# Optimization experiments

Measured on AMD Instinct MI355X. Metric: run time of the kernel, lower is better.

The kernel has to match this reference:

```python
import jax, jax.numpy as jnp
import numpy as np

# NF4 codebook (bitsandbytes nf4 data type, 16 levels)
NF4_TABLE = np.array([
    -1.0, -0.6961928009986877, -0.5250730514526367, -0.39491748809814453,
    -0.28444138169288635, -0.18477343022823334, -0.09105003625154495, 0.0,
    0.07958029955625534, 0.16093020141124725, 0.24611230194568634,
    0.33791524171829224, 0.44070982933044434, 0.5626170039176941,
    0.7229568362236023, 1.0], dtype=np.float32)

BLOCKSIZE = 64
SCALING = 32.0 / 16.0  # lora_alpha / r


def setup_inputs() -> dict:
    key = jax.random.key(0)
    k1, k2, k3, k4, k5 = jax.random.split(key, 5)
    tokens, in_f, out_f, r = 256, 4096, 11008, 16
    x = jax.random.normal(k1, (tokens, in_f), dtype=jnp.float32)
    q_codes = jax.random.randint(k2, (out_f, in_f), 0, 16, dtype=jnp.int32)
    absmax = jax.random.uniform(k3, (out_f, in_f // BLOCKSIZE), dtype=jnp.float32)
    lora_A = jax.random.normal(k4, (r, in_f), dtype=jnp.float32) * (1.0 / np.sqrt(in_f))
    lora_B = jax.random.normal(k5, (out_f, r), dtype=jnp.float32) * 0.02
    return {"x": x, "q_codes": q_codes, "absmax": absmax,
            "lora_A": lora_A, "lora_B": lora_B}


def reference(x, q_codes, absmax, lora_A, lora_B):
    out_f, in_f = q_codes.shape
    nf4 = jnp.asarray(NF4_TABLE, dtype=x.dtype)
    # Dequantize: codebook lookup, then per-block absmax scale.
    W = nf4[q_codes].reshape(out_f, in_f // BLOCKSIZE, BLOCKSIZE)
    W = (W * absmax[:, :, None]).reshape(out_f, in_f)  # [out_f, in_f]
    # Base 4-bit linear (no bias in bnb Linear4bit default here).
    base = x @ W.T  # [tokens, out_f]
    # LoRA path: dropout p=0 is identity in eval; scaling = alpha/r.
    lora = (x @ lora_A.T) @ lora_B.T  # [tokens, r] -> [tokens, out_f]
    return base + lora * jnp.asarray(SCALING, dtype=x.dtype)
```

## Files before the change

kernel.cpp:

```cpp
#include <hip/hip_runtime.h>
#include <hip/hip_fp16.h>

typedef unsigned int uint;
typedef unsigned short ushort;

typedef __attribute__((ext_vector_type(8))) _Float16 f16x8;
typedef __attribute__((ext_vector_type(4))) float f32x4;

#define TOK 256
#define OUTF 11008
#define INF 4096
#define BM 256
#define BN 64
#define NT2 172

__device__ __constant__ float NF4_TBL[16] = {
    -1.0f, -0.6961928009986877f, -0.5250730514526367f, -0.39491748809814453f,
    -0.28444138169288635f, -0.18477343022823334f, -0.09105003625154495f, 0.0f,
    0.07958029955625534f, 0.16093020141124725f, 0.24611230194568634f,
    0.33791524171829224f, 0.44070982933044434f, 0.5626170039176941f,
    0.7229568362236023f, 1.0f};

__device__ __forceinline__ ushort f2h(float f) {
  return __half_as_ushort(__float2half(f));
}

__device__ __forceinline__ void async_cp16(const void* g, void* l) {
  __builtin_amdgcn_global_load_lds(
      (const __attribute__((address_space(1))) uint*)g,
      (__attribute__((address_space(3))) uint*)l, 16, 0, 0);
}

__device__ __forceinline__ float nf4v(int c, int tbits) {
  return __int_as_float(__builtin_amdgcn_ds_bpermute(c << 2, tbits));
}

__global__ void prep_kernel(const float4* __restrict__ x4, ushort4* __restrict__ xh4,
                            const float4* __restrict__ lB4, ushort4* __restrict__ lBh4,
                            const int4* __restrict__ qc4, uint* __restrict__ q4) {
  const int stride = gridDim.x * blockDim.x;
  const int t0 = blockIdx.x * blockDim.x + threadIdx.x;
  for (int i = t0; i < OUTF * (INF / 8); i += stride) {
    int4 a = qc4[(size_t)i * 2];
    int4 b = qc4[(size_t)i * 2 + 1];
    uint p = (uint)(a.x & 15) | ((uint)(a.y & 15) << 4) | ((uint)(a.z & 15) << 8) |
             ((uint)(a.w & 15) << 12) | ((uint)(b.x & 15) << 16) |
             ((uint)(b.y & 15) << 20) | ((uint)(b.z & 15) << 24) |
             ((uint)(b.w & 15) << 28);
    q4[i] = p;
  }
  for (int i = t0; i < TOK * INF / 4; i += stride) {
    float4 v = x4[i];
    ushort4 o;
    o.x = f2h(v.x); o.y = f2h(v.y); o.z = f2h(v.z); o.w = f2h(v.w);
    xh4[i] = o;
  }
  for (int i = t0; i < OUTF * 16; i += stride) {
    int n = i >> 4, jq = i & 15;
    ushort4 o = {0, 0, 0, 0};
    if (jq < 4) {
      float4 v = lB4[n * 4 + jq];
      o.x = f2h(v.x); o.y = f2h(v.y); o.z = f2h(v.z); o.w = f2h(v.w);
    }
    lBh4[i] = o;
  }
}

__global__ __launch_bounds__(1024)
void xa_kernel(const float* __restrict__ x, const float* __restrict__ lA,
               ushort* __restrict__ xa2) {
  const int m = blockIdx.x;
  const int t = threadIdx.x;
  const float4* x4 = (const float4*)(x + (size_t)m * INF);
  const float4* lA4 = (const float4*)lA;
  float4 xv = x4[t];
  float acc[16];
#pragma unroll
  for (int j = 0; j < 16; ++j) {
    float4 a = lA4[j * (INF / 4) + t];
    acc[j] = xv.x * a.x + xv.y * a.y + xv.z * a.z + xv.w * a.w;
  }
#pragma unroll
  for (int j = 0; j < 16; ++j)
#pragma unroll
    for (int s = 32; s > 0; s >>= 1) acc[j] += __shfl_xor(acc[j], s, 64);
  __shared__ float red[16][16];
  const int w = t >> 6, l = t & 63;
  if (l == 0) {
#pragma unroll
    for (int j = 0; j < 16; ++j) red[w][j] = acc[j];
  }
  __syncthreads();
  if (t < 64) {
    ushort v = 0;
    if (t < 16) {
      float s = 0.f;
#pragma unroll
      for (int w2 = 0; w2 < 16; ++w2) s += red[w2][t];
      v = f2h(2.0f * s);
    }
    xa2[m * 64 + t] = v;
  }
}

__global__ __launch_bounds__(256, 3)
void gemm_kernel(const uint* __restrict__ q4, const float* __restrict__ am,
                 const ushort* __restrict__ xh, const ushort* __restrict__ lBh,
                 const ushort* __restrict__ xa2, float* __restrict__ dest, int nst) {
  __shared__ ushort Abuf[BM * 64];
  __shared__ ushort Bbuf[64 * 64];
  __shared__ float Qax[1024];

  const int tid = threadIdx.x;
  const int w = tid >> 6;
  const int l = tid & 63;
  const int chunk = l >> 4;
  const int rlo = l & 15;
  const int split = blockIdx.x / NT2;
  const int ntile = blockIdx.x - split * NT2;
  const int n0 = ntile * BN;
  const int kb0 = split * nst;

  const int tbits = __float_as_int(NF4_TBL[l & 15]);

  const int arow = w * 8 + (l >> 3);
  const int acol = ((l & 7) ^ (l >> 3)) << 3;
  int aoff[2][4];
#pragma unroll
  for (int ks2 = 0; ks2 < 2; ++ks2) {
    const int cc = ks2 * 4 + chunk;
#pragma unroll
    for (int mt = 0; mt < 4; ++mt)
      aoff[ks2][mt] = (w * 64 + mt * 16 + rlo) * 64 + ((cc ^ (l & 7)) << 3);
  }

  const int qr = tid >> 2;
  const int oc2 = (tid & 3) << 1;
  const uint* qb = q4 + (size_t)(n0 + qr) * (INF / 8) + (size_t)kb0 * 8 + oc2;
  const int bd0 = qr * 64 + ((oc2 ^ (qr & 7)) << 3);
  const int bd1 = qr * 64 + (((oc2 + 1) ^ (qr & 7)) << 3);

  int boff[2][4];
#pragma unroll
  for (int ks2 = 0; ks2 < 2; ++ks2)
#pragma unroll
    for (int nt = 0; nt < 4; ++nt)
      boff[ks2][nt] = (nt * 16 + rlo) * 64 + (((ks2 * 4 + chunk) ^ (rlo & 7)) << 3);

  f32x4 acc[4][4];
#pragma unroll
  for (int mt = 0; mt < 4; ++mt)
#pragma unroll
    for (int nt = 0; nt < 4; ++nt) acc[mt][nt] = (f32x4){0.f, 0.f, 0.f, 0.f};

  if (w == 0) {
#pragma unroll
    for (int j = 0; j < 4; ++j)
      async_cp16(am + (size_t)(n0 + l) * 64 + kb0 + j * 4, (char*)Qax + j * 1024);
  }
#pragma unroll
  for (int i = 0; i < 8; ++i) {
    const ushort* g = xh + (size_t)(i * 32 + arow) * INF + kb0 * 64 + acol;
    async_cp16(g, &Abuf[(i * 256 + w * 64) * 8]);
  }
  uint2 qreg = *(const uint2*)qb;

  for (int s = 0; s < nst; ++s) {
    __syncthreads();

    const int sl = s & 15;
    const __half2 ax2 = __float2half2_rn(Qax[(sl >> 2) * 256 + qr * 4 + (sl & 3)]);
    {
      const uint q0 = qreg.x, q1 = qreg.y;
      union { __half2 h[4]; uint4 u; } r0, r1;
      r0.h[0] = __hmul2(__floats2half2_rn(nf4v(q0 & 15, tbits), nf4v((q0 >> 4) & 15, tbits)), ax2);
      r0.h[1] = __hmul2(__floats2half2_rn(nf4v((q0 >> 8) & 15, tbits), nf4v((q0 >> 12) & 15, tbits)), ax2);
      r0.h[2] = __hmul2(__floats2half2_rn(nf4v((q0 >> 16) & 15, tbits), nf4v((q0 >> 20) & 15, tbits)), ax2);
      r0.h[3] = __hmul2(__floats2half2_rn(nf4v((q0 >> 24) & 15, tbits), nf4v(q0 >> 28, tbits)), ax2);
      r1.h[0] = __hmul2(__floats2half2_rn(nf4v(q1 & 15, tbits), nf4v((q1 >> 4) & 15, tbits)), ax2);
      r1.h[1] = __hmul2(__floats2half2_rn(nf4v((q1 >> 8) & 15, tbits), nf4v((q1 >> 12) & 15, tbits)), ax2);
      r1.h[2] = __hmul2(__floats2half2_rn(nf4v((q1 >> 16) & 15, tbits), nf4v((q1 >> 20) & 15, tbits)), ax2);
      r1.h[3] = __hmul2(__floats2half2_rn(nf4v((q1 >> 24) & 15, tbits), nf4v(q1 >> 28, tbits)), ax2);
      *(uint4*)&Bbuf[bd0] = r0.u;
      *(uint4*)&Bbuf[bd1] = r1.u;
    }
    f16x8 areg[2][4];
#pragma unroll
    for (int ks2 = 0; ks2 < 2; ++ks2)
#pragma unroll
      for (int mt = 0; mt < 4; ++mt) areg[ks2][mt] = *(const f16x8*)&Abuf[aoff[ks2][mt]];

    __syncthreads();

    if (s + 1 < nst) {
      const int kb = kb0 + s + 1;
#pragma unroll
      for (int i = 0; i < 8; ++i) {
        const ushort* g = xh + (size_t)(i * 32 + arow) * INF + kb * 64 + acol;
        async_cp16(g, &Abuf[(i * 256 + w * 64) * 8]);
      }
      qreg = *(const uint2*)(qb + (s + 1) * 8);
      if (((s + 1) & 15) == 0 && w == 0) {
#pragma unroll
        for (int j = 0; j < 4; ++j)
          async_cp16(am + (size_t)(n0 + l) * 64 + kb0 + s + 1 + j * 4, (char*)Qax + j * 1024);
      }
    }

#pragma unroll
    for (int ks2 = 0; ks2 < 2; ++ks2) {
      f16x8 b[4];
#pragma unroll
      for (int nt = 0; nt < 4; ++nt) b[nt] = *(const f16x8*)&Bbuf[boff[ks2][nt]];
#pragma unroll
      for (int mt = 0; mt < 4; ++mt)
#pragma unroll
        for (int nt = 0; nt < 4; ++nt)
          acc[mt][nt] = __builtin_amdgcn_mfma_f32_16x16x32_f16(areg[ks2][mt], b[nt], acc[mt][nt], 0, 0, 0);
    }
  }

  if (split == 0) {
    f16x8 a_l[4], b_l[4];
#pragma unroll
    for (int mt = 0; mt < 4; ++mt)
      a_l[mt] = *(const f16x8*)(xa2 + (size_t)(w * 64 + mt * 16 + rlo) * 64 + chunk * 8);
#pragma unroll
    for (int nt = 0; nt < 4; ++nt)
      b_l[nt] = *(const f16x8*)(lBh + (size_t)(n0 + nt * 16 + rlo) * 64 + chunk * 8);
#pragma unroll
    for (int mt = 0; mt < 4; ++mt)
#pragma unroll
      for (int nt = 0; nt < 4; ++nt)
        acc[mt][nt] = __builtin_amdgcn_mfma_f32_16x16x32_f16(a_l[mt], b_l[nt], acc[mt][nt], 0, 0, 0);
  }

  float* dst = dest + (size_t)split * TOK * OUTF;
#pragma unroll
  for (int mt = 0; mt < 4; ++mt) {
#pragma unroll
    for (int nt = 0; nt < 4; ++nt) {
      int c = n0 + nt * 16 + rlo;
#pragma unroll
      for (int r = 0; r < 4; ++r) {
        int row = w * 64 + mt * 16 + chunk * 4 + r;
        dst[(size_t)row * OUTF + c] = acc[mt][nt][r];
      }
    }
  }
}

__global__ void reduce_kernel(const float4* __restrict__ part, float4* __restrict__ out,
                              int ks) {
  const int QN = TOK * OUTF / 4;
  int i = blockIdx.x * blockDim.x + threadIdx.x;
  if (i < QN) {
    float4 s = part[i];
    for (int s2 = 1; s2 < ks; ++s2) {
      float4 p = part[(size_t)s2 * QN + i];
      s.x += p.x; s.y += p.y; s.z += p.z; s.w += p.w;
    }
    out[i] = s;
  }
}

extern "C" void kernel_launch(void* const* d_in, const int* in_sizes, int n_in,
                              void* d_out, int out_size, void* d_ws, size_t ws_size,
                              hipStream_t stream) {
  const float* x = (const float*)d_in[0];
  const int* qc = (const int*)d_in[1];
  const float* am = (const float*)d_in[2];
  const float* lA = (const float*)d_in[3];
  const float* lB = (const float*)d_in[4];
  float* out = (float*)d_out;

  const size_t off_lB = (size_t)TOK * INF * 2;
  const size_t off_xa2 = off_lB + (size_t)OUTF * 64 * 2;
  const size_t off_q4 = off_xa2 + (size_t)TOK * 64 * 2;
  const size_t off_part = off_q4 + (size_t)OUTF * (INF / 8) * 4;
  const size_t part_bytes = (size_t)TOK * OUTF * 4;

  ushort* xh = (ushort*)d_ws;
  ushort* lBh = (ushort*)((char*)d_ws + off_lB);
  ushort* xa2 = (ushort*)((char*)d_ws + off_xa2);
  uint* q4 = (uint*)((char*)d_ws + off_q4);
  float* part = (float*)((char*)d_ws + off_part);

  int ks = 1;
  if (ws_size >= off_part + 4 * part_bytes) ks = 4;
  else if (ws_size >= off_part + 2 * part_bytes) ks = 2;
  float* dest = (ks == 1) ? out : part;

  prep_kernel<<<2048, 256, 0, stream>>>((const float4*)x, (ushort4*)xh,
                                        (const float4*)lB, (ushort4*)lBh,
                                        (const int4*)qc, q4);
  xa_kernel<<<TOK, 1024, 0, stream>>>(x, lA, xa2);
  gemm_kernel<<<NT2 * ks, 256, 0, stream>>>(q4, am, xh, lBh, xa2, dest, 64 / ks);
  if (ks > 1)
    reduce_kernel<<<(TOK * OUTF / 4 + 255) / 256, 256, 0, stream>>>((const float4*)part,
                                                                    (float4*)out, ks);
}
```

Before: 323.8 us.

## Pre-swizzle x into MFMA fragment order and double-buffer dequantized B tiles

The prep kernel now writes fp16 x in the exact per-lane MFMA fragment layout, so the GEMM loads A operands straight from global memory into registers. This removes the LDS A buffer and its async copies. The main loop is software-pipelined with two register sets for A and two LDS B buffers, so dequantizing the next tile overlaps with MFMA on the current one, and each step needs one lightweight barrier instead of two. All absmax values for the tile are loaded up front, and MFMA sections get raised priority. In exchange, register pressure rises (launch bounds drop to 2 waves), every A load goes to global memory or cache, and the absmax load ignores the kb0 offset when split > 0, which may be a correctness bug.

Measured after the change: 327.4 us. No clear change (+1.1%).

```diff
diff --git a/kernel.cpp b/kernel.cpp
--- a/kernel.cpp
+++ b/kernel.cpp
@@ -35,7 +35,12 @@
   return __int_as_float(__builtin_amdgcn_ds_bpermute(c << 2, tbits));
 }
 
-__global__ void prep_kernel(const float4* __restrict__ x4, ushort4* __restrict__ xh4,
+__device__ __forceinline__ void step_barrier() {
+  asm volatile("s_waitcnt lgkmcnt(0)" ::: "memory");
+  __builtin_amdgcn_s_barrier();
+}
+
+__global__ void prep_kernel(const float* __restrict__ x, uint4* __restrict__ xf4,
                             const float4* __restrict__ lB4, ushort4* __restrict__ lBh4,
                             const int4* __restrict__ qc4, uint* __restrict__ q4) {
   const int stride = gridDim.x * blockDim.x;
@@ -49,11 +54,21 @@
              ((uint)(b.w & 15) << 28);
     q4[i] = p;
   }
-  for (int i = t0; i < TOK * INF / 4; i += stride) {
-    float4 v = x4[i];
-    ushort4 o;
-    o.x = f2h(v.x); o.y = f2h(v.y); o.z = f2h(v.z); o.w = f2h(v.w);
-    xh4[i] = o;
+  for (int f = t0; f < TOK * INF / 8; f += stride) {
+    int l = f & 63;
+    int rlo = l & 15, chunk = l >> 4;
+    int ms = (f >> 6) & 7;
+    int mt = ms >> 1, ks2 = ms & 1;
+    int w = (f >> 9) & 3;
+    int kb = f >> 11;
+    int m = w * 64 + mt * 16 + rlo;
+    int k0 = kb * 64 + (ks2 * 4 + chunk) * 8;
+    const float4* src = (const float4*)(x + (size_t)m * INF + k0);
+    float4 v0 = src[0], v1 = src[1];
+    union { ushort4 h[2]; uint4 u; } pk;
+    pk.h[0].x = f2h(v0.x); pk.h[0].y = f2h(v0.y); pk.h[0].z = f2h(v0.z); pk.h[0].w = f2h(v0.w);
+    pk.h[1].x = f2h(v1.x); pk.h[1].y = f2h(v1.y); pk.h[1].z = f2h(v1.z); pk.h[1].w = f2h(v1.w);
+    xf4[f] = pk.u;
   }
   for (int i = t0; i < OUTF * 16; i += stride) {
     int n = i >> 4, jq = i & 15;
@@ -103,13 +118,12 @@
   }
 }
 
-__global__ __launch_bounds__(256, 3)
+__global__ __launch_bounds__(256, 2)
 void gemm_kernel(const uint* __restrict__ q4, const float* __restrict__ am,
-                 const ushort* __restrict__ xh, const ushort* __restrict__ lBh,
+                 const ushort* __restrict__ xf, const ushort* __restrict__ lBh,
                  const ushort* __restrict__ xa2, float* __restrict__ dest, int nst) {
-  __shared__ ushort Abuf[BM * 64];
-  __shared__ ushort Bbuf[64 * 64];
-  __shared__ float Qax[1024];
+  __shared__ ushort Bbuf[2][64 * 64];
+  __shared__ float Qax[4096];
 
   const int tid = threadIdx.x;
   const int w = tid >> 6;
@@ -123,17 +137,6 @@
 
   const int tbits = __float_as_int(NF4_TBL[l & 15]);
 
-  const int arow = w * 8 + (l >> 3);
-  const int acol = ((l & 7) ^ (l >> 3)) << 3;
-  int aoff[2][4];
-#pragma unroll
-  for (int ks2 = 0; ks2 < 2; ++ks2) {
-    const int cc = ks2 * 4 + chunk;
-#pragma unroll
-    for (int mt = 0; mt < 4; ++mt)
-      aoff[ks2][mt] = (w * 64 + mt * 16 + rlo) * 64 + ((cc ^ (l & 7)) << 3);
-  }
-
   const int qr = tid >> 2;
   const int oc2 = (tid & 3) << 1;
   const uint* qb = q4 + (size_t)(n0 + qr) * (INF / 8) + (size_t)kb0 * 8 + oc2;
@@ -153,71 +156,76 @@
 #pragma unroll
     for (int nt = 0; nt < 4; ++nt) acc[mt][nt] = (f32x4){0.f, 0.f, 0.f, 0.f};
 
-  if (w == 0) {
-#pragma unroll
-    for (int j = 0; j < 4; ++j)
-      async_cp16(am + (size_t)(n0 + l) * 64 + kb0 + j * 4, (char*)Qax + j * 1024);
-  }
-#pragma unroll
-  for (int i = 0; i < 8; ++i) {
-    const ushort* g = xh + (size_t)(i * 32 + arow) * INF + kb0 * 64 + acol;
-    async_cp16(g, &Abuf[(i * 256 + w * 64) * 8]);
-  }
-  uint2 qreg = *(const uint2*)qb;
-
-  for (int s = 0; s < nst; ++s) {
-    __syncthreads();
-
-    const int sl = s & 15;
-    const __half2 ax2 = __float2half2_rn(Qax[(sl >> 2) * 256 + qr * 4 + (sl & 3)]);
-    {
-      const uint q0 = qreg.x, q1 = qreg.y;
-      union { __half2 h[4]; uint4 u; } r0, r1;
-      r0.h[0] = __hmul2(__floats2half2_rn(nf4v(q0 & 15, tbits), nf4v((q0 >> 4) & 15, tbits)), ax2);
-      r0.h[1] = __hmul2(__floats2half2_rn(nf4v((q0 >> 8) & 15, tbits), nf4v((q0 >> 12) & 15, tbits)), ax2);
-      r0.h[2] = __hmul2(__floats2half2_rn(nf4v((q0 >> 16) & 15, tbits), nf4v((q0 >> 20) & 15, tbits)), ax2);
-      r0.h[3] = __hmul2(__floats2half2_rn(nf4v((q0 >> 24) & 15, tbits), nf4v(q0 >> 28, tbits)), ax2);
-      r1.h[0] = __hmul2(__floats2half2_rn(nf4v(q1 & 15, tbits), nf4v((q1 >> 4) & 15, tbits)), ax2);
-      r1.h[1] = __hmul2(__floats2half2_rn(nf4v((q1 >> 8) & 15, tbits), nf4v((q1 >> 12) & 15, tbits)), ax2);
-      r1.h[2] = __hmul2(__floats2half2_rn(nf4v((q1 >> 16) & 15, tbits), nf4v((q1 >> 20) & 15, tbits)), ax2);
-      r1.h[3] = __hmul2(__floats2half2_rn(nf4v((q1 >> 24) & 15, tbits), nf4v(q1 >> 28, tbits)), ax2);
-      *(uint4*)&Bbuf[bd0] = r0.u;
-      *(uint4*)&Bbuf[bd1] = r1.u;
-    }
-    f16x8 areg[2][4];
-#pragma unroll
-    for (int ks2 = 0; ks2 < 2; ++ks2)
-#pragma unroll
-      for (int mt = 0; mt < 4; ++mt) areg[ks2][mt] = *(const f16x8*)&Abuf[aoff[ks2][mt]];
-
-    __syncthreads();
-
-    if (s + 1 < nst) {
-      const int kb = kb0 + s + 1;
-#pragma unroll
-      for (int i = 0; i < 8; ++i) {
-        const ushort* g = xh + (size_t)(i * 32 + arow) * INF + kb * 64 + acol;
-        async_cp16(g, &Abuf[(i * 256 + w * 64) * 8]);
-      }
-      qreg = *(const uint2*)(qb + (s + 1) * 8);
-      if (((s + 1) & 15) == 0 && w == 0) {
-#pragma unroll
-        for (int j = 0; j < 4; ++j)
-          async_cp16(am + (size_t)(n0 + l) * 64 + kb0 + s + 1 + j * 4, (char*)Qax + j * 1024);
-      }
-    }
-
+  auto loadA = [&](f16x8 ar[2][4], int kb) {
+    const ushort* base = xf + ((size_t)kb * 4 + w) * 4096 + (size_t)l * 8;
+#pragma unroll
+    for (int mt = 0; mt < 4; ++mt)
+#pragma unroll
+      for (int ks2 = 0; ks2 < 2; ++ks2)
+        ar[ks2][mt] = *(const f16x8*)(base + (mt * 2 + ks2) * 512);
+  };
+
+  auto dequantF = [&](uint2 q, int kbt, ushort* bb) {
+    const __half2 ax2 = __float2half2_rn(Qax[(kbt >> 2) * 256 + qr * 4 + (kbt & 3)]);
+    const uint q0 = q.x, q1 = q.y;
+    union { __half2 h[4]; uint4 u; } r0, r1;
+    r0.h[0] = __hmul2(__floats2half2_rn(nf4v(q0 & 15, tbits), nf4v((q0 >> 4) & 15, tbits)), ax2);
+    r0.h[1] = __hmul2(__floats2half2_rn(nf4v((q0 >> 8) & 15, tbits), nf4v((q0 >> 12) & 15, tbits)), ax2);
+    r0.h[2] = __hmul2(__floats2half2_rn(nf4v((q0 >> 16) & 15, tbits), nf4v((q0 >> 20) & 15, tbits)), ax2);
+    r0.h[3] = __hmul2(__floats2half2_rn(nf4v((q0 >> 24) & 15, tbits), nf4v(q0 >> 28, tbits)), ax2);
+    r1.h[0] = __hmul2(__floats2half2_rn(nf4v(q1 & 15, tbits), nf4v((q1 >> 4) & 15, tbits)), ax2);
+    r1.h[1] = __hmul2(__floats2half2_rn(nf4v((q1 >> 8) & 15, tbits), nf4v((q1 >> 12) & 15, tbits)), ax2);
+    r1.h[2] = __hmul2(__floats2half2_rn(nf4v((q1 >> 16) & 15, tbits), nf4v((q1 >> 20) & 15, tbits)), ax2);
+    r1.h[3] = __hmul2(__floats2half2_rn(nf4v((q1 >> 24) & 15, tbits), nf4v(q1 >> 28, tbits)), ax2);
+    *(uint4*)&bb[bd0] = r0.u;
+    *(uint4*)&bb[bd1] = r1.u;
+  };
+
+  auto compute = [&](f16x8 ar[2][4], const ushort* bb) {
+    __builtin_amdgcn_s_setprio(1);
 #pragma unroll
     for (int ks2 = 0; ks2 < 2; ++ks2) {
       f16x8 b[4];
 #pragma unroll
-      for (int nt = 0; nt < 4; ++nt) b[nt] = *(const f16x8*)&Bbuf[boff[ks2][nt]];
+      for (int nt = 0; nt < 4; ++nt) b[nt] = *(const f16x8*)&bb[boff[ks2][nt]];
 #pragma unroll
       for (int mt = 0; mt < 4; ++mt)
 #pragma unroll
         for (int nt = 0; nt < 4; ++nt)
-          acc[mt][nt] = __builtin_amdgcn_mfma_f32_16x16x32_f16(areg[ks2][mt], b[nt], acc[mt][nt], 0, 0, 0);
-    }
+          acc[mt][nt] = __builtin_amdgcn_mfma_f32_16x16x32_f16(ar[ks2][mt], b[nt], acc[mt][nt], 0, 0, 0);
+    }
+    __builtin_amdgcn_s_setprio(0);
+  };
+
+  if (w == 0) {
+#pragma unroll
+    for (int j = 0; j < 16; ++j)
+      async_cp16(am + (size_t)(n0 + l) * 64 + j * 4, (char*)Qax + j * 1024);
+  }
+  f16x8 arA[2][4], arB[2][4];
+  loadA(arA, kb0);
+  loadA(arB, kb0 + 1);
+  uint2 qA = *(const uint2*)qb;
+  uint2 qB = *(const uint2*)(qb + 8);
+  __syncthreads();
+  dequantF(qA, kb0, Bbuf[0]);
+  step_barrier();
+
+  for (int s = 0; s < nst; s += 2) {
+    compute(arA, Bbuf[0]);
+    if (s + 1 < nst) dequantF(qB, kb0 + s + 1, Bbuf[1]);
+    if (s + 2 < nst) {
+      loadA(arA, kb0 + s + 2);
+      qA = *(const uint2*)(qb + (size_t)(s + 2) * 8);
+    }
+    step_barrier();
+    compute(arB, Bbuf[1]);
+    if (s + 2 < nst) dequantF(qA, kb0 + s + 2, Bbuf[0]);
+    if (s + 3 < nst) {
+      loadA(arB, kb0 + s + 3);
+      qB = *(const uint2*)(qb + (size_t)(s + 3) * 8);
+    }
+    step_barrier();
   }
 
   if (split == 0) {
@@ -280,7 +288,7 @@
   const size_t off_part = off_q4 + (size_t)OUTF * (INF / 8) * 4;
   const size_t part_bytes = (size_t)TOK * OUTF * 4;
 
-  ushort* xh = (ushort*)d_ws;
+  ushort* xf = (ushort*)d_ws;
   ushort* lBh = (ushort*)((char*)d_ws + off_lB);
   ushort* xa2 = (ushort*)((char*)d_ws + off_xa2);
   uint* q4 = (uint*)((char*)d_ws + off_q4);
@@ -291,11 +299,10 @@
   else if (ws_size >= off_part + 2 * part_bytes) ks = 2;
   float* dest = (ks == 1) ? out : part;
 
-  prep_kernel<<<2048, 256, 0, stream>>>((const float4*)x, (ushort4*)xh,
-                                        (const float4*)lB, (ushort4*)lBh,
-                                        (const int4*)qc, q4);
+  prep_kernel<<<2048, 256, 0, stream>>>(x, (uint4*)xf, (const float4*)lB,
+                                        (ushort4*)lBh, (const int4*)qc, q4);
   xa_kernel<<<TOK, 1024, 0, stream>>>(x, lA, xa2);
-  gemm_kernel<<<NT2 * ks, 256, 0, stream>>>(q4, am, xh, lBh, xa2, dest, 64 / ks);
+  gemm_kernel<<<NT2 * ks, 256, 0, stream>>>(q4, am, xf, lBh, xa2, dest, 64 / ks);
   if (ks > 1)
     reduce_kernel<<<(TOK * OUTF / 4 + 255) / 256, 256, 0, stream>>>((const float4*)part,
                                                                     (float4*)out, ks);
```
